# Kernel tuning notes

Hardware: AMD Instinct MI355X
Metric: run time of the kernel (lower is better)

## Reference

```python
import jax, jax.numpy as jnp
import numpy as np

N = 100000      # nodes
E = 1600000     # edges
G = 1024        # graphs in batch
NF = 9          # atom features (OGB AtomEncoder)
V = 128         # vocab per atom feature
H = 128         # hidden_dim
L = 3           # num_graph_layers
OUT = 10        # output_dim
BN_EPS = 1e-5


def setup_inputs() -> dict:
    key = jax.random.key(0)
    ks = jax.random.split(key, 12)
    x = jax.random.randint(ks[0], (N, NF), 0, V, dtype=jnp.int32)
    edge_index = jax.random.randint(ks[1], (2, E), 0, N, dtype=jnp.int32)
    batch = jnp.sort(jax.random.randint(ks[2], (N,), 0, G, dtype=jnp.int32))
    emb = jax.random.normal(ks[3], (NF, V, H), dtype=jnp.float32) * 0.05
    Ws = jax.random.normal(ks[4], (L, H, H), dtype=jnp.float32) * (1.0 / np.sqrt(H))
    bs = jnp.zeros((L, H), dtype=jnp.float32)
    gamma = jnp.ones((L - 1, H), dtype=jnp.float32)
    beta = jnp.zeros((L - 1, H), dtype=jnp.float32)
    run_mean = jax.random.normal(ks[5], (L - 1, H), dtype=jnp.float32) * 0.1
    run_var = jax.random.uniform(ks[6], (L - 1, H), minval=0.5, maxval=1.5, dtype=jnp.float32)
    W_clf = jax.random.normal(ks[7], (H, OUT), dtype=jnp.float32) * (1.0 / np.sqrt(H))
    b_clf = jnp.zeros((OUT,), dtype=jnp.float32)
    return {"x": x, "edge_index": edge_index, "batch": batch, "emb": emb,
            "Ws": Ws, "bs": bs, "gamma": gamma, "beta": beta,
            "run_mean": run_mean, "run_var": run_var,
            "W_clf": W_clf, "b_clf": b_clf}


def reference(x, edge_index, batch, emb, Ws, bs, gamma, beta, run_mean, run_var, W_clf, b_clf):
    # Eval-mode forward: dropout = identity, BatchNorm uses running stats.
    src, dst = edge_index[0], edge_index[1]
    # GCN symmetric normalization with self-loops: deg = 1 + in-degree
    deg = jax.ops.segment_sum(jnp.ones((E,), jnp.float32), dst, num_segments=N) + 1.0
    dinv = jax.lax.rsqrt(deg)                 # [N]
    norm_e = dinv[src] * dinv[dst]            # [E] edge coefficient
    norm_self = dinv * dinv                   # [N] self-loop coefficient

    # AtomEncoder: sum of per-feature embedding lookups -> [N, H]
    h = emb[jnp.arange(NF)[None, :], x].sum(axis=1)

    for i in range(L):
        hw = h @ Ws[i]                                                       # [N, H]
        h = (jax.ops.segment_sum(hw[src] * norm_e[:, None], dst, num_segments=N)
             + hw * norm_self[:, None] + bs[i])                              # GCNConv
        if i < L - 1:
            h = (h - run_mean[i]) * (gamma[i] * jax.lax.rsqrt(run_var[i] + BN_EPS)) + beta[i]
            h = jax.nn.relu(h)

    # global mean pool over graphs
    counts = jax.ops.segment_sum(jnp.ones((N,), jnp.float32), batch, num_segments=G)
    pooled = jax.ops.segment_sum(h, batch, num_segments=G) / jnp.maximum(counts, 1.0)[:, None]
    return pooled @ W_clf + b_clf             # [G, OUT]
```

## Files before the change

### kernel.cpp

```cpp
#include <hip/hip_runtime.h>
#include <hip/hip_bf16.h>
#include <hip/hip_fp16.h>

#define NN 100000
#define EE 1600000
#define GG 1024
#define NF 9
#define VV 128
#define HH 128
#define LL 3
#define OUTD 10
#define BN_EPS 1e-5f
#define NB_SCAN 98
#define NBUCK 196
#define BCAP 12288
#define CHUNK 4096
#define NB64 1563

typedef __attribute__((ext_vector_type(8))) short short8;
typedef __attribute__((ext_vector_type(8))) _Float16 half8;
typedef __attribute__((ext_vector_type(4))) float f32x4;

__device__ inline unsigned short f2bf(float x) {
    unsigned u = __float_as_uint(x);
    unsigned r = (u + 0x7fffu + ((u >> 16) & 1u)) >> 16;
    return (unsigned short)r;
}
__device__ inline float bf2f(unsigned short b) { return __uint_as_float(((unsigned)b) << 16); }

__device__ inline void mix8(float a[8], const uint4& r, float nm) {
    asm("v_fma_mix_f32 %0, %8, %12, %0 op_sel:[0,0,0] op_sel_hi:[1,0,0]\n\t"
        "v_fma_mix_f32 %1, %8, %12, %1 op_sel:[1,0,0] op_sel_hi:[1,0,0]\n\t"
        "v_fma_mix_f32 %2, %9, %12, %2 op_sel:[0,0,0] op_sel_hi:[1,0,0]\n\t"
        "v_fma_mix_f32 %3, %9, %12, %3 op_sel:[1,0,0] op_sel_hi:[1,0,0]\n\t"
        "v_fma_mix_f32 %4, %10, %12, %4 op_sel:[0,0,0] op_sel_hi:[1,0,0]\n\t"
        "v_fma_mix_f32 %5, %10, %12, %5 op_sel:[1,0,0] op_sel_hi:[1,0,0]\n\t"
        "v_fma_mix_f32 %6, %11, %12, %6 op_sel:[0,0,0] op_sel_hi:[1,0,0]\n\t"
        "v_fma_mix_f32 %7, %11, %12, %7 op_sel:[1,0,0] op_sel_hi:[1,0,0]"
        : "+v"(a[0]), "+v"(a[1]), "+v"(a[2]), "+v"(a[3]),
          "+v"(a[4]), "+v"(a[5]), "+v"(a[6]), "+v"(a[7])
        : "v"(r.x), "v"(r.y), "v"(r.z), "v"(r.w), "v"(nm));
}

__device__ inline void fma4(float4& a, const float4 r, float nm) {
    a.x = fmaf(r.x, nm, a.x); a.y = fmaf(r.y, nm, a.y);
    a.z = fmaf(r.z, nm, a.z); a.w = fmaf(r.w, nm, a.w);
}

__global__ __launch_bounds__(256) void split_kernel(const int* __restrict__ src,
                                                    const int* __restrict__ dst,
                                                    int* __restrict__ bcur,
                                                    int* __restrict__ bucket_edges) {
    __shared__ int lcnt[256], loff[256], lcur[256], gbase[256], sh[256];
    __shared__ int stage[CHUNK];
    __shared__ unsigned char stageb[CHUNK];
    int tid = threadIdx.x;
    int cs = blockIdx.x * CHUNK;
    int n = min(CHUNK, EE - cs);
    lcnt[tid] = 0;
    __syncthreads();
    for (int i = tid; i < n; i += 256)
        atomicAdd(&lcnt[dst[cs + i] >> 9], 1);
    __syncthreads();
    int val = lcnt[tid];
    sh[tid] = val; __syncthreads();
    for (int d = 1; d < 256; d <<= 1) {
        int t = (tid >= d) ? sh[tid - d] : 0;
        __syncthreads();
        sh[tid] += t;
        __syncthreads();
    }
    loff[tid] = sh[tid] - val;
    lcur[tid] = sh[tid] - val;
    __syncthreads();
    for (int i = tid; i < n; i += 256) {
        int d = dst[cs + i], s = src[cs + i];
        int b = d >> 9;
        int p = atomicAdd(&lcur[b], 1);
        stage[p] = (s << 9) | (d & 511);
        stageb[p] = (unsigned char)b;
    }
    if (val > 0) gbase[tid] = atomicAdd(&bcur[tid], val);
    __syncthreads();
    for (int i = tid; i < n; i += 256) {
        int b = stageb[i];
        bucket_edges[(size_t)b * BCAP + gbase[b] + (i - loff[b])] = stage[i];
    }
}

__global__ __launch_bounds__(256) void bhist_kernel(const int* __restrict__ bcur,
                                                    const int* __restrict__ bucket_edges,
                                                    int* __restrict__ cnt) {
    __shared__ int lc[512];
    int b = blockIdx.x, tid = threadIdx.x;
    lc[tid] = 0; lc[tid + 256] = 0;
    __syncthreads();
    int n = bcur[b];
    const int* be = bucket_edges + (size_t)b * BCAP;
    for (int i = tid; i < n; i += 256) atomicAdd(&lc[be[i] & 511], 1);
    __syncthreads();
    int node = b * 512 + tid;
    if (node < NN) cnt[node] = lc[tid];
    node += 256;
    if (node < NN) cnt[node] = lc[tid + 256];
}

__global__ void scanA_kernel(const int* __restrict__ cnt, int* __restrict__ bsum,
                             float* __restrict__ dinv) {
    __shared__ int sh[256];
    int tid = threadIdx.x;
    int base = blockIdx.x * 1024 + tid * 4;
    int s = 0;
#pragma unroll
    for (int i = 0; i < 4; ++i) {
        int idx = base + i;
        if (idx < NN) {
            int c = cnt[idx];
            s += c;
            dinv[idx] = rsqrtf(1.0f + (float)c);
        }
    }
    sh[tid] = s; __syncthreads();
    for (int d = 128; d > 0; d >>= 1) { if (tid < d) sh[tid] += sh[tid + d]; __syncthreads(); }
    if (tid == 0) bsum[blockIdx.x] = sh[0];
}

__global__ void scanB_kernel(int* __restrict__ bsum) {
    __shared__ int sh[128];
    int tid = threadIdx.x;
    int v = (tid < NB_SCAN) ? bsum[tid] : 0;
    sh[tid] = v; __syncthreads();
    for (int d = 1; d < 128; d <<= 1) {
        int t = (tid >= d) ? sh[tid - d] : 0;
        __syncthreads();
        sh[tid] += t;
        __syncthreads();
    }
    if (tid < NB_SCAN) bsum[tid] = sh[tid] - v;
}

__global__ void scanC_kernel(const int* __restrict__ cnt, const int* __restrict__ bsum,
                             int* __restrict__ row_ptr) {
    __shared__ int sh[256];
    int tid = threadIdx.x;
    int base = blockIdx.x * 1024 + tid * 4;
    int v[4];
#pragma unroll
    for (int i = 0; i < 4; ++i) { int idx = base + i; v[i] = (idx < NN) ? cnt[idx] : 0; }
    int tsum = v[0] + v[1] + v[2] + v[3];
    sh[tid] = tsum; __syncthreads();
    for (int d = 1; d < 256; d <<= 1) {
        int t = (tid >= d) ? sh[tid - d] : 0;
        __syncthreads();
        sh[tid] += t;
        __syncthreads();
    }
    int excl = sh[tid] - tsum + bsum[blockIdx.x];
#pragma unroll
    for (int i = 0; i < 4; ++i) {
        int idx = base + i;
        if (idx < NN) row_ptr[idx] = excl;
        excl += v[i];
    }
    if (blockIdx.x == 0 && tid == 0) row_ptr[NN] = EE;
}

__global__ __launch_bounds__(256) void cscatter_kernel(const int* __restrict__ bcur,
                                                       const int* __restrict__ bucket_edges,
                                                       const int* __restrict__ row_ptr,
                                                       const float* __restrict__ dinv,
                                                       int2* __restrict__ col) {
    __shared__ int lcur[512];
    int b = blockIdx.x, tid = threadIdx.x;
    int node0 = b * 512;
#pragma unroll
    for (int k = 0; k < 2; ++k) {
        int j = tid + k * 256;
        int node = node0 + j;
        if (node < NN) lcur[j] = row_ptr[node];
    }
    __syncthreads();
    int n = bcur[b];
    const int* be = bucket_edges + (size_t)b * BCAP;
    for (int i = tid; i < n; i += 256) {
        int w = be[i];
        int j = w & 511;
        int s = (int)((unsigned)w >> 9);
        int p = atomicAdd(&lcur[j], 1);
        float nm = dinv[s] * dinv[node0 + j];
        col[p] = make_int2(s, __float_as_int(nm));
    }
}

__global__ void wconv_kernel(const float* __restrict__ Ws,
                             unsigned short* __restrict__ WThi,
                             unsigned short* __restrict__ WTlo) {
    int id = blockIdx.x * 256 + threadIdx.x;
    if (id >= LL * HH * HH) return;
    int layer = id >> 14;
    int rem = id & (HH * HH - 1);
    int k = rem >> 7, n = rem & 127;
    float w = Ws[id];
    unsigned short hi = f2bf(w);
    float lo = w - bf2f(hi);
    WThi[(size_t)layer * HH * HH + n * HH + k] = hi;
    WTlo[(size_t)layer * HH * HH + n * HH + k] = f2bf(lo);
}

__global__ __launch_bounds__(256) void prep_clf_kernel(const float* __restrict__ Wc,
        const float* __restrict__ b2,
        _Float16* __restrict__ WcThi, _Float16* __restrict__ WcTlo,
        float* __restrict__ bb2) {
    int tid = threadIdx.x;
    for (int id = tid; id < 16 * HH; id += 256) {
        int n = id >> 7, k = id & 127;
        float w = (n < OUTD) ? Wc[k * OUTD + n] : 0.f;
        _Float16 hi = (_Float16)w;
        float lo = w - (float)hi;
        WcThi[id] = hi;
        WcTlo[id] = (_Float16)lo;
    }
    if (tid < OUTD) {
        float s = 0.f;
        for (int c = 0; c < HH; ++c) s += b2[c] * Wc[c * OUTD + tid];
        bb2[tid] = s;
    }
}

__global__ __launch_bounds__(256) void enc_mm_kernel(const int* __restrict__ x,
        const float* __restrict__ emb,
        const unsigned short* __restrict__ WThi, const unsigned short* __restrict__ WTlo,
        __half* __restrict__ hw_out) {
    __shared__ __align__(16) unsigned short lh[32][136];
    __shared__ __align__(16) unsigned short ll[32][136];
    int tid = threadIdx.x;
    int nloc = tid >> 3;
    int seg = tid & 7;
    int nodebase = blockIdx.x * 32;
    int n = nodebase + nloc;
    float s[16];
#pragma unroll
    for (int i = 0; i < 16; ++i) s[i] = 0.f;
#pragma unroll
    for (int f = 0; f < NF; ++f) {
        int idx = x[n * NF + f];
        const float4* ep = (const float4*)(emb + ((size_t)(f * VV + idx)) * HH + seg * 16);
#pragma unroll
        for (int q = 0; q < 4; ++q) {
            float4 e = ep[q];
            s[q * 4 + 0] += e.x; s[q * 4 + 1] += e.y;
            s[q * 4 + 2] += e.z; s[q * 4 + 3] += e.w;
        }
    }
#pragma unroll
    for (int q = 0; q < 4; ++q) {
        ushort4 oh, ol;
        oh.x = f2bf(s[q * 4 + 0]); ol.x = f2bf(s[q * 4 + 0] - bf2f(oh.x));
        oh.y = f2bf(s[q * 4 + 1]); ol.y = f2bf(s[q * 4 + 1] - bf2f(oh.y));
        oh.z = f2bf(s[q * 4 + 2]); ol.z = f2bf(s[q * 4 + 2] - bf2f(oh.z));
        oh.w = f2bf(s[q * 4 + 3]); ol.w = f2bf(s[q * 4 + 3] - bf2f(oh.w));
        *(ushort4*)&lh[nloc][seg * 16 + q * 4] = oh;
        *(ushort4*)&ll[nloc][seg * 16 + q * 4] = ol;
    }
    __syncthreads();
    int wave = tid >> 6, lane = tid & 63;
    int quad = lane >> 4, m = lane & 15;
    f32x4 acc[2][2] = {};
    int kq = quad * 8;
#pragma unroll
    for (int t = 0; t < 4; ++t) {
        int k0 = t * 32 + kq;
        short8 a0h = *(const short8*)&lh[m][k0];
        short8 a0l = *(const short8*)&ll[m][k0];
        short8 a1h = *(const short8*)&lh[16 + m][k0];
        short8 a1l = *(const short8*)&ll[16 + m][k0];
#pragma unroll
        for (int c = 0; c < 2; ++c) {
            int ct = wave * 2 + c;
            short8 bh = *(const short8*)(WThi + (size_t)(ct * 16 + m) * HH + k0);
            short8 bl = *(const short8*)(WTlo + (size_t)(ct * 16 + m) * HH + k0);
            acc[0][c] = __builtin_amdgcn_mfma_f32_16x16x32_bf16(a0h, bh, acc[0][c], 0, 0, 0);
            acc[0][c] = __builtin_amdgcn_mfma_f32_16x16x32_bf16(a0l, bh, acc[0][c], 0, 0, 0);
            acc[0][c] = __builtin_amdgcn_mfma_f32_16x16x32_bf16(a0h, bl, acc[0][c], 0, 0, 0);
            acc[1][c] = __builtin_amdgcn_mfma_f32_16x16x32_bf16(a1h, bh, acc[1][c], 0, 0, 0);
            acc[1][c] = __builtin_amdgcn_mfma_f32_16x16x32_bf16(a1l, bh, acc[1][c], 0, 0, 0);
            acc[1][c] = __builtin_amdgcn_mfma_f32_16x16x32_bf16(a1h, bl, acc[1][c], 0, 0, 0);
        }
    }
#pragma unroll
    for (int c = 0; c < 2; ++c) {
        int colx = (wave * 2 + c) * 16 + m;
#pragma unroll
        for (int rt = 0; rt < 2; ++rt) {
            int r0 = nodebase + rt * 16 + quad * 4;
#pragma unroll
            for (int reg = 0; reg < 4; ++reg)
                hw_out[(size_t)(r0 + reg) * HH + colx] = __float2half(acc[rt][c][reg]);
        }
    }
}

__device__ inline void gather_node(const uint4* __restrict__ hw4,
                                   const int2* __restrict__ col,
                                   int start, int end, int c4,
                                   float a[8], float b[8]) {
    int e = start;
    for (; e + 4 <= end; e += 4) {
        unsigned long long w0 = *(const unsigned long long*)&col[e];
        unsigned long long w1 = *(const unsigned long long*)&col[e + 1];
        unsigned long long w2 = *(const unsigned long long*)&col[e + 2];
        unsigned long long w3 = *(const unsigned long long*)&col[e + 3];
        uint4 r0 = hw4[(size_t)(unsigned)(w0 & 0xffffffffu) * 16 + c4];
        uint4 r1 = hw4[(size_t)(unsigned)(w1 & 0xffffffffu) * 16 + c4];
        uint4 r2 = hw4[(size_t)(unsigned)(w2 & 0xffffffffu) * 16 + c4];
        uint4 r3 = hw4[(size_t)(unsigned)(w3 & 0xffffffffu) * 16 + c4];
        mix8(a, r0, __int_as_float((int)(unsigned)(w0 >> 32)));
        mix8(b, r1, __int_as_float((int)(unsigned)(w1 >> 32)));
        mix8(a, r2, __int_as_float((int)(unsigned)(w2 >> 32)));
        mix8(b, r3, __int_as_float((int)(unsigned)(w3 >> 32)));
    }
    if (e < end) {
        int last = end - 1;
        int e1 = min(e + 1, last), e2 = min(e + 2, last), e3 = min(e + 3, last);
        unsigned long long w0 = *(const unsigned long long*)&col[e];
        unsigned long long w1 = *(const unsigned long long*)&col[e1];
        unsigned long long w2 = *(const unsigned long long*)&col[e2];
        unsigned long long w3 = *(const unsigned long long*)&col[e3];
        float n0 = __int_as_float((int)(unsigned)(w0 >> 32));
        float n1 = (e + 1 < end) ? __int_as_float((int)(unsigned)(w1 >> 32)) : 0.f;
        float n2 = (e + 2 < end) ? __int_as_float((int)(unsigned)(w2 >> 32)) : 0.f;
        float n3 = (e + 3 < end) ? __int_as_float((int)(unsigned)(w3 >> 32)) : 0.f;
        uint4 r0 = hw4[(size_t)(unsigned)(w0 & 0xffffffffu) * 16 + c4];
        uint4 r1 = hw4[(size_t)(unsigned)(w1 & 0xffffffffu) * 16 + c4];
        uint4 r2 = hw4[(size_t)(unsigned)(w2 & 0xffffffffu) * 16 + c4];
        uint4 r3 = hw4[(size_t)(unsigned)(w3 & 0xffffffffu) * 16 + c4];
        mix8(a, r0, n0);
        mix8(b, r1, n1);
        mix8(a, r2, n2);
        mix8(b, r3, n3);
    }
}

__global__ __launch_bounds__(512) void agg_mm_kernel(const __half* __restrict__ hw_in,
    const int* __restrict__ row_ptr, const int2* __restrict__ col,
    const float* __restrict__ dinv,
    const float* __restrict__ bias, const float* __restrict__ gamma,
    const float* __restrict__ beta, const float* __restrict__ rmean,
    const float* __restrict__ rvar,
    const unsigned short* __restrict__ WThi, const unsigned short* __restrict__ WTlo,
    __half* __restrict__ hw_out) {
    __shared__ __align__(16) unsigned short lh[32][136];
    __shared__ __align__(16) unsigned short ll[32][136];
    int wave = threadIdx.x >> 6;
    int lane = threadIdx.x & 63;
    int grp = lane >> 4;
    int c4 = lane & 15;
    int nodebase = blockIdx.x * 32;
    const uint4* hw4 = (const uint4*)hw_in;

    int v = nodebase + wave * 4 + grp;
    int start = row_ptr[v], end = row_ptr[v + 1];
    float a[8] = {}, b[8] = {};
    gather_node(hw4, col, start, end, c4, a, b);

    {
        float dv = dinv[v];
        uint4 r = hw4[(size_t)v * 16 + c4];
        mix8(a, r, dv * dv);
    }
#pragma unroll
    for (int i = 0; i < 8; ++i) a[i] += b[i];

    int ch = c4 * 8;
#pragma unroll
    for (int i = 0; i < 8; ++i) a[i] += bias[ch + i];
#pragma unroll
    for (int i = 0; i < 8; ++i) {
        int c = ch + i;
        float sc = gamma[c] * rsqrtf(rvar[c] + BN_EPS);
        a[i] = fmaxf((a[i] - rmean[c]) * sc + beta[c], 0.f);
    }
    int rloc = wave * 4 + grp;
    ushort4 oh0, oh1, ol0, ol1;
    oh0.x = f2bf(a[0]); ol0.x = f2bf(a[0] - bf2f(oh0.x));
    oh0.y = f2bf(a[1]); ol0.y = f2bf(a[1] - bf2f(oh0.y));
    oh0.z = f2bf(a[2]); ol0.z = f2bf(a[2] - bf2f(oh0.z));
    oh0.w = f2bf(a[3]); ol0.w = f2bf(a[3] - bf2f(oh0.w));
    oh1.x = f2bf(a[4]); ol1.x = f2bf(a[4] - bf2f(oh1.x));
    oh1.y = f2bf(a[5]); ol1.y = f2bf(a[5] - bf2f(oh1.y));
    oh1.z = f2bf(a[6]); ol1.z = f2bf(a[6] - bf2f(oh1.z));
    oh1.w = f2bf(a[7]); ol1.w = f2bf(a[7] - bf2f(oh1.w));
    *(ushort4*)&lh[rloc][ch]     = oh0;
    *(ushort4*)&lh[rloc][ch + 4] = oh1;
    *(ushort4*)&ll[rloc][ch]     = ol0;
    *(ushort4*)&ll[rloc][ch + 4] = ol1;

    __syncthreads();
    int quad = lane >> 4, m = lane & 15;
    f32x4 acc[2] = {};
    int kq = quad * 8;
    int ct = wave;
#pragma unroll
    for (int t = 0; t < 4; ++t) {
        int k0 = t * 32 + kq;
        short8 a0h = *(const short8*)&lh[m][k0];
        short8 a0l = *(const short8*)&ll[m][k0];
        short8 a1h = *(const short8*)&lh[16 + m][k0];
        short8 a1l = *(const short8*)&ll[16 + m][k0];
        short8 bh = *(const short8*)(WThi + (size_t)(ct * 16 + m) * HH + k0);
        short8 bl = *(const short8*)(WTlo + (size_t)(ct * 16 + m) * HH + k0);
        acc[0] = __builtin_amdgcn_mfma_f32_16x16x32_bf16(a0h, bh, acc[0], 0, 0, 0);
        acc[0] = __builtin_amdgcn_mfma_f32_16x16x32_bf16(a0l, bh, acc[0], 0, 0, 0);
        acc[0] = __builtin_amdgcn_mfma_f32_16x16x32_bf16(a0h, bl, acc[0], 0, 0, 0);
        acc[1] = __builtin_amdgcn_mfma_f32_16x16x32_bf16(a1h, bh, acc[1], 0, 0, 0);
        acc[1] = __builtin_amdgcn_mfma_f32_16x16x32_bf16(a1l, bh, acc[1], 0, 0, 0);
        acc[1] = __builtin_amdgcn_mfma_f32_16x16x32_bf16(a1h, bl, acc[1], 0, 0, 0);
    }
    int colx = ct * 16 + m;
#pragma unroll
    for (int rt = 0; rt < 2; ++rt) {
        int r0 = nodebase + rt * 16 + quad * 4;
#pragma unroll
        for (int reg = 0; reg < 4; ++reg)
            hw_out[(size_t)(r0 + reg) * HH + colx] = __float2half(acc[rt][reg]);
    }
}

__global__ __launch_bounds__(256) void yproj_kernel(const __half* __restrict__ hw_in,
        const _Float16* __restrict__ WcThi, const _Float16* __restrict__ WcTlo,
        float* __restrict__ y) {
    int tid = threadIdx.x;
    int wv = tid >> 6, lane = tid & 63;
    int quad = lane >> 4, m = lane & 15;
    int nodebase = blockIdx.x * 64 + wv * 16;
    int an = min(nodebase + m, NN - 1);
    f32x4 acc = {};
#pragma unroll
    for (int t = 0; t < 4; ++t) {
        int k0 = t * 32 + quad * 8;
        half8 a  = *(const half8*)(hw_in + (size_t)an * HH + k0);
        half8 bh = *(const half8*)(WcThi + m * HH + k0);
        half8 bl = *(const half8*)(WcTlo + m * HH + k0);
        acc = __builtin_amdgcn_mfma_f32_16x16x32_f16(a, bh, acc, 0, 0, 0);
        acc = __builtin_amdgcn_mfma_f32_16x16x32_f16(a, bl, acc, 0, 0, 0);
    }
#pragma unroll
    for (int reg = 0; reg < 4; ++reg) {
        int node = nodebase + quad * 4 + reg;
        if (node < NN) y[(size_t)node * 16 + m] = acc[reg];
    }
}

__global__ __launch_bounds__(256) void agg_pool10_kernel(const float* __restrict__ y,
    const int* __restrict__ row_ptr, const int2* __restrict__ col,
    const float* __restrict__ dinv, const int* __restrict__ batch,
    float* __restrict__ pooled) {
    __shared__ __align__(16) float lz[64][16];
    __shared__ int bg[64];
    int tid = threadIdx.x;
    int g4 = tid >> 2;
    int c = tid & 3;
    int nodebase = blockIdx.x * 64;
    int v = nodebase + g4;
    int vc = min(v, NN - 1);
    int start = row_ptr[vc];
    int end = (v < NN) ? row_ptr[vc + 1] : start;
    const float4* y4 = (const float4*)y;
    float4 a = {0.f, 0.f, 0.f, 0.f}, b = {0.f, 0.f, 0.f, 0.f};
    int e = start;
    for (; e + 4 <= end; e += 4) {
        unsigned long long w0 = *(const unsigned long long*)&col[e];
        unsigned long long w1 = *(const unsigned long long*)&col[e + 1];
        unsigned long long w2 = *(const unsigned long long*)&col[e + 2];
        unsigned long long w3 = *(const unsigned long long*)&col[e + 3];
        float4 r0 = y4[(size_t)(unsigned)(w0 & 0xffffffffu) * 4 + c];
        float4 r1 = y4[(size_t)(unsigned)(w1 & 0xffffffffu) * 4 + c];
        float4 r2 = y4[(size_t)(unsigned)(w2 & 0xffffffffu) * 4 + c];
        float4 r3 = y4[(size_t)(unsigned)(w3 & 0xffffffffu) * 4 + c];
        fma4(a, r0, __int_as_float((int)(unsigned)(w0 >> 32)));
        fma4(b, r1, __int_as_float((int)(unsigned)(w1 >> 32)));
        fma4(a, r2, __int_as_float((int)(unsigned)(w2 >> 32)));
        fma4(b, r3, __int_as_float((int)(unsigned)(w3 >> 32)));
    }
    if (e < end) {
        int last = end - 1;
        int e1 = min(e + 1, last), e2 = min(e + 2, last), e3 = min(e + 3, last);
        unsigned long long w0 = *(const unsigned long long*)&col[e];
        unsigned long long w1 = *(const unsigned long long*)&col[e1];
        unsigned long long w2 = *(const unsigned long long*)&col[e2];
        unsigned long long w3 = *(const unsigned long long*)&col[e3];
        float n0 = __int_as_float((int)(unsigned)(w0 >> 32));
        float n1 = (e + 1 < end) ? __int_as_float((int)(unsigned)(w1 >> 32)) : 0.f;
        float n2 = (e + 2 < end) ? __int_as_float((int)(unsigned)(w2 >> 32)) : 0.f;
        float n3 = (e + 3 < end) ? __int_as_float((int)(unsigned)(w3 >> 32)) : 0.f;
        float4 r0 = y4[(size_t)(unsigned)(w0 & 0xffffffffu) * 4 + c];
        float4 r1 = y4[(size_t)(unsigned)(w1 & 0xffffffffu) * 4 + c];
        float4 r2 = y4[(size_t)(unsigned)(w2 & 0xffffffffu) * 4 + c];
        float4 r3 = y4[(size_t)(unsigned)(w3 & 0xffffffffu) * 4 + c];
        fma4(a, r0, n0);
        fma4(b, r1, n1);
        fma4(a, r2, n2);
        fma4(b, r3, n3);
    }
    if (v < NN) {
        float dv = dinv[v];
        float4 r = y4[(size_t)v * 4 + c];
        fma4(a, r, dv * dv);
    }
    a.x += b.x; a.y += b.y; a.z += b.z; a.w += b.w;
    *(float4*)&lz[g4][c * 4] = a;
    if (c == 0) bg[g4] = batch[vc];
    __syncthreads();
    int ch = tid & 15;
    int rh = tid >> 4;
    int r0i = rh * 4;
    int curg = bg[r0i];
    float run = 0.f;
    for (int r = r0i; r < r0i + 4; ++r) {
        int gg = bg[r];
        if (gg != curg) {
            atomicAdd(&pooled[(size_t)curg * 16 + ch], run);
            run = 0.f; curg = gg;
        }
        run += lz[r][ch];
    }
    atomicAdd(&pooled[(size_t)curg * 16 + ch], run);
}

__global__ __launch_bounds__(256) void finalize_kernel(const float* __restrict__ pooled,
    const int* __restrict__ batch, const float* __restrict__ bb2,
    const float* __restrict__ bc, float* __restrict__ out) {
    int id = blockIdx.x * 256 + threadIdx.x;
    if (id >= GG * 16) return;
    int g = id >> 4, o = id & 15;
    if (o >= OUTD) return;
    int lo = 0, hi = NN;
    while (lo < hi) { int mid = (lo + hi) >> 1; if (batch[mid] < g) lo = mid + 1; else hi = mid; }
    int s0 = lo;
    lo = 0; hi = NN;
    int g1 = g + 1;
    while (lo < hi) { int mid = (lo + hi) >> 1; if (batch[mid] < g1) lo = mid + 1; else hi = mid; }
    int cnt = lo - s0;
    float r = pooled[(size_t)g * 16 + o] / fmaxf((float)cnt, 1.0f);
    out[(size_t)g * OUTD + o] = r + ((cnt > 0) ? bb2[o] : 0.f) + bc[o];
}

extern "C" void kernel_launch(void* const* d_in, const int* in_sizes, int n_in,
                              void* d_out, int out_size, void* d_ws, size_t ws_size,
                              hipStream_t stream) {
    const int*   x      = (const int*)d_in[0];
    const int*   eidx   = (const int*)d_in[1];
    const int*   batch  = (const int*)d_in[2];
    const float* emb    = (const float*)d_in[3];
    const float* Ws     = (const float*)d_in[4];
    const float* bs     = (const float*)d_in[5];
    const float* gamma  = (const float*)d_in[6];
    const float* beta   = (const float*)d_in[7];
    const float* rmean  = (const float*)d_in[8];
    const float* rvar   = (const float*)d_in[9];
    const float* Wclf   = (const float*)d_in[10];
    const float* bclf   = (const float*)d_in[11];
    float* out = (float*)d_out;

    const int* e_src = eidx;
    const int* e_dst = eidx + EE;

    char* ws = (char*)d_ws;
    size_t off = 0;
    auto take = [&](size_t bytes) -> void* {
        void* p = ws + off;
        off = (off + bytes + 255) & ~(size_t)255;
        return p;
    };
    float* dinv     = (float*)take((size_t)NN * 4);
    int*   cnt      = (int*)  take((size_t)NN * 4);
    int*   row_ptr  = (int*)  take((size_t)(NN + 1) * 4);
    int*   bsum     = (int*)  take((size_t)NB_SCAN * 4);
    int*   bcur     = (int*)  take((size_t)256 * 4);
    int*   bucket_edges = (int*)take((size_t)NBUCK * BCAP * 4);
    int2*  col      = (int2*) take((size_t)EE * 8);
    __half* hwA     = (__half*)take((size_t)NN * HH * 2);
    __half* hwB     = (__half*)take((size_t)NN * HH * 2);
    float* y        = (float*)take((size_t)NN * 16 * 4);
    float* pooled   = (float*)take((size_t)GG * 16 * 4);
    unsigned short* WThi = (unsigned short*)take((size_t)LL * HH * HH * 2);
    unsigned short* WTlo = (unsigned short*)take((size_t)LL * HH * HH * 2);
    _Float16* WcThi = (_Float16*)take((size_t)16 * HH * 2);
    _Float16* WcTlo = (_Float16*)take((size_t)16 * HH * 2);
    float* bb2      = (float*)take((size_t)16 * 4);

    hipMemsetAsync(bcur, 0, 256 * 4, stream);
    hipMemsetAsync(pooled, 0, (size_t)GG * 16 * 4, stream);

    split_kernel<<<(EE + CHUNK - 1) / CHUNK, 256, 0, stream>>>(e_src, e_dst, bcur, bucket_edges);
    bhist_kernel<<<NBUCK, 256, 0, stream>>>(bcur, bucket_edges, cnt);
    scanA_kernel<<<NB_SCAN, 256, 0, stream>>>(cnt, bsum, dinv);
    scanB_kernel<<<1, 128, 0, stream>>>(bsum);
    scanC_kernel<<<NB_SCAN, 256, 0, stream>>>(cnt, bsum, row_ptr);
    cscatter_kernel<<<NBUCK, 256, 0, stream>>>(bcur, bucket_edges, row_ptr, dinv, col);
    wconv_kernel<<<(LL * HH * HH + 255) / 256, 256, 0, stream>>>(Ws, WThi, WTlo);
    prep_clf_kernel<<<1, 256, 0, stream>>>(Wclf, bs + 2 * HH, WcThi, WcTlo, bb2);

    enc_mm_kernel<<<NN / 32, 256, 0, stream>>>(x, emb, WThi, WTlo, hwA);
    agg_mm_kernel<<<NN / 32, 512, 0, stream>>>(hwA, row_ptr, col, dinv,
        bs, gamma, beta, rmean, rvar,
        WThi + (size_t)1 * HH * HH, WTlo + (size_t)1 * HH * HH, hwB);
    agg_mm_kernel<<<NN / 32, 512, 0, stream>>>(hwB, row_ptr, col, dinv,
        bs + HH, gamma + HH, beta + HH, rmean + HH, rvar + HH,
        WThi + (size_t)2 * HH * HH, WTlo + (size_t)2 * HH * HH, hwA);
    yproj_kernel<<<NB64, 256, 0, stream>>>(hwA, WcThi, WcTlo, y);
    agg_pool10_kernel<<<NB64, 256, 0, stream>>>(y, row_ptr, col, dinv, batch, pooled);
    finalize_kernel<<<(GG * 16 + 255) / 256, 256, 0, stream>>>(pooled, batch, bb2, bclf, out);
}
```

Baseline: 412.0 us.

## Fuse classifier projection into last GCN layer and store projected features in fp16

```diff
diff --git a/kernel.cpp b/kernel.cpp
--- a/kernel.cpp
+++ b/kernel.cpp
@@ -11,14 +11,12 @@
 #define LL 3
 #define OUTD 10
 #define BN_EPS 1e-5f
-#define NB_SCAN 98
 #define NBUCK 196
 #define BCAP 12288
 #define CHUNK 4096
-#define NB64 1563
+#define NB128 782
 
 typedef __attribute__((ext_vector_type(8))) short short8;
-typedef __attribute__((ext_vector_type(8))) _Float16 half8;
 typedef __attribute__((ext_vector_type(4))) float f32x4;
 
 __device__ inline unsigned short f2bf(float x) {
@@ -42,11 +40,6 @@
         : "v"(r.x), "v"(r.y), "v"(r.z), "v"(r.w), "v"(nm));
 }
 
-__device__ inline void fma4(float4& a, const float4 r, float nm) {
-    a.x = fmaf(r.x, nm, a.x); a.y = fmaf(r.y, nm, a.y);
-    a.z = fmaf(r.z, nm, a.z); a.w = fmaf(r.w, nm, a.w);
-}
-
 __global__ __launch_bounds__(256) void split_kernel(const int* __restrict__ src,
                                                     const int* __restrict__ dst,
                                                     int* __restrict__ bcur,
@@ -90,8 +83,11 @@
 
 __global__ __launch_bounds__(256) void bhist_kernel(const int* __restrict__ bcur,
                                                     const int* __restrict__ bucket_edges,
-                                                    int* __restrict__ cnt) {
+                                                    int* __restrict__ cnt,
+                                                    float* __restrict__ dinv,
+                                                    int* __restrict__ bsum) {
     __shared__ int lc[512];
+    __shared__ int sh[256];
     int b = blockIdx.x, tid = threadIdx.x;
     lc[tid] = 0; lc[tid + 256] = 0;
     __syncthreads();
@@ -100,68 +96,47 @@
     for (int i = tid; i < n; i += 256) atomicAdd(&lc[be[i] & 511], 1);
     __syncthreads();
     int node = b * 512 + tid;
-    if (node < NN) cnt[node] = lc[tid];
-    node += 256;
-    if (node < NN) cnt[node] = lc[tid + 256];
-}
-
-__global__ void scanA_kernel(const int* __restrict__ cnt, int* __restrict__ bsum,
-                             float* __restrict__ dinv) {
+    int c0 = lc[tid], c1 = lc[tid + 256];
+    int s = 0;
+    if (node < NN) { cnt[node] = c0; dinv[node] = rsqrtf(1.0f + (float)c0); s += c0; }
+    if (node + 256 < NN) { cnt[node + 256] = c1; dinv[node + 256] = rsqrtf(1.0f + (float)c1); s += c1; }
+    sh[tid] = s; __syncthreads();
+    for (int d = 128; d > 0; d >>= 1) { if (tid < d) sh[tid] += sh[tid + d]; __syncthreads(); }
+    if (tid == 0) bsum[b] = sh[0];
+}
+
+__global__ void scanB_kernel(int* __restrict__ bsum) {
     __shared__ int sh[256];
     int tid = threadIdx.x;
-    int base = blockIdx.x * 1024 + tid * 4;
-    int s = 0;
-#pragma unroll
-    for (int i = 0; i < 4; ++i) {
-        int idx = base + i;
-        if (idx < NN) {
-            int c = cnt[idx];
-            s += c;
-            dinv[idx] = rsqrtf(1.0f + (float)c);
-        }
-    }
-    sh[tid] = s; __syncthreads();
-    for (int d = 128; d > 0; d >>= 1) { if (tid < d) sh[tid] += sh[tid + d]; __syncthreads(); }
-    if (tid == 0) bsum[blockIdx.x] = sh[0];
-}
-
-__global__ void scanB_kernel(int* __restrict__ bsum) {
-    __shared__ int sh[128];
-    int tid = threadIdx.x;
-    int v = (tid < NB_SCAN) ? bsum[tid] : 0;
+    int v = (tid < NBUCK) ? bsum[tid] : 0;
     sh[tid] = v; __syncthreads();
-    for (int d = 1; d < 128; d <<= 1) {
-        int t = (tid >= d) ? sh[tid - d] : 0;
-        __syncthreads();
-        sh[tid] += t;
-        __syncthreads();
-    }
-    if (tid < NB_SCAN) bsum[tid] = sh[tid] - v;
-}
-
-__global__ void scanC_kernel(const int* __restrict__ cnt, const int* __restrict__ bsum,
-                             int* __restrict__ row_ptr) {
-    __shared__ int sh[256];
-    int tid = threadIdx.x;
-    int base = blockIdx.x * 1024 + tid * 4;
-    int v[4];
-#pragma unroll
-    for (int i = 0; i < 4; ++i) { int idx = base + i; v[i] = (idx < NN) ? cnt[idx] : 0; }
-    int tsum = v[0] + v[1] + v[2] + v[3];
-    sh[tid] = tsum; __syncthreads();
     for (int d = 1; d < 256; d <<= 1) {
         int t = (tid >= d) ? sh[tid - d] : 0;
         __syncthreads();
         sh[tid] += t;
         __syncthreads();
     }
-    int excl = sh[tid] - tsum + bsum[blockIdx.x];
-#pragma unroll
-    for (int i = 0; i < 4; ++i) {
-        int idx = base + i;
-        if (idx < NN) row_ptr[idx] = excl;
-        excl += v[i];
-    }
+    if (tid < NBUCK) bsum[tid] = sh[tid] - v;
+}
+
+__global__ void scanC_kernel(const int* __restrict__ cnt, const int* __restrict__ bsum,
+                             int* __restrict__ row_ptr) {
+    __shared__ int sh[256];
+    int tid = threadIdx.x;
+    int base = blockIdx.x * 512 + tid * 2;
+    int v0 = (base < NN) ? cnt[base] : 0;
+    int v1 = (base + 1 < NN) ? cnt[base + 1] : 0;
+    int ts = v0 + v1;
+    sh[tid] = ts; __syncthreads();
+    for (int d = 1; d < 256; d <<= 1) {
+        int t = (tid >= d) ? sh[tid - d] : 0;
+        __syncthreads();
+        sh[tid] += t;
+        __syncthreads();
+    }
+    int excl = sh[tid] - ts + bsum[blockIdx.x];
+    if (base < NN) row_ptr[base] = excl;
+    if (base + 1 < NN) row_ptr[base + 1] = excl + v0;
     if (blockIdx.x == 0 && tid == 0) row_ptr[NN] = EE;
 }
 
@@ -192,38 +167,41 @@
     }
 }
 
-__global__ void wconv_kernel(const float* __restrict__ Ws,
-                             unsigned short* __restrict__ WThi,
-                             unsigned short* __restrict__ WTlo) {
+__global__ __launch_bounds__(256) void wprep_kernel(const float* __restrict__ Ws,
+        const float* __restrict__ Wc, const float* __restrict__ b2,
+        unsigned short* __restrict__ WThi, unsigned short* __restrict__ WTlo,
+        unsigned short* __restrict__ WcThi, unsigned short* __restrict__ WcTlo,
+        float* __restrict__ bb2) {
     int id = blockIdx.x * 256 + threadIdx.x;
-    if (id >= LL * HH * HH) return;
-    int layer = id >> 14;
-    int rem = id & (HH * HH - 1);
-    int k = rem >> 7, n = rem & 127;
-    float w = Ws[id];
-    unsigned short hi = f2bf(w);
-    float lo = w - bf2f(hi);
-    WThi[(size_t)layer * HH * HH + n * HH + k] = hi;
-    WTlo[(size_t)layer * HH * HH + n * HH + k] = f2bf(lo);
-}
-
-__global__ __launch_bounds__(256) void prep_clf_kernel(const float* __restrict__ Wc,
-        const float* __restrict__ b2,
-        _Float16* __restrict__ WcThi, _Float16* __restrict__ WcTlo,
-        float* __restrict__ bb2) {
-    int tid = threadIdx.x;
-    for (int id = tid; id < 16 * HH; id += 256) {
-        int n = id >> 7, k = id & 127;
-        float w = (n < OUTD) ? Wc[k * OUTD + n] : 0.f;
-        _Float16 hi = (_Float16)w;
-        float lo = w - (float)hi;
-        WcThi[id] = hi;
-        WcTlo[id] = (_Float16)lo;
-    }
-    if (tid < OUTD) {
-        float s = 0.f;
-        for (int c = 0; c < HH; ++c) s += b2[c] * Wc[c * OUTD + tid];
-        bb2[tid] = s;
+    if (id < LL * HH * HH) {
+        int layer = id >> 14;
+        int rem = id & (HH * HH - 1);
+        int k = rem >> 7, n = rem & 127;
+        float w = Ws[id];
+        unsigned short hi = f2bf(w);
+        float lo = w - bf2f(hi);
+        WThi[(size_t)layer * HH * HH + n * HH + k] = hi;
+        WTlo[(size_t)layer * HH * HH + n * HH + k] = f2bf(lo);
+    }
+    if (blockIdx.x == 0) {
+        int tid = threadIdx.x;
+        const float* W2 = Ws + (size_t)2 * HH * HH;
+        for (int i = tid; i < 16 * HH; i += 256) {
+            int n = i >> 7, k = i & 127;
+            float s = 0.f;
+            if (n < OUTD) {
+                for (int j = 0; j < HH; ++j)
+                    s += W2[k * HH + j] * Wc[j * OUTD + n];
+            }
+            unsigned short hi = f2bf(s);
+            WcThi[i] = hi;
+            WcTlo[i] = f2bf(s - bf2f(hi));
+        }
+        if (tid < OUTD) {
+            float s = 0.f;
+            for (int c = 0; c < HH; ++c) s += b2[c] * Wc[c * OUTD + tid];
+            bb2[tid] = s;
+        }
     }
 }
 
@@ -341,6 +319,7 @@
     }
 }
 
+template<bool DO_PROJ>
 __global__ __launch_bounds__(512) void agg_mm_kernel(const __half* __restrict__ hw_in,
     const int* __restrict__ row_ptr, const int2* __restrict__ col,
     const float* __restrict__ dinv,
@@ -348,7 +327,9 @@
     const float* __restrict__ beta, const float* __restrict__ rmean,
     const float* __restrict__ rvar,
     const unsigned short* __restrict__ WThi, const unsigned short* __restrict__ WTlo,
-    __half* __restrict__ hw_out) {
+    __half* __restrict__ hw_out,
+    const unsigned short* __restrict__ WcThi, const unsigned short* __restrict__ WcTlo,
+    __half* __restrict__ y_out) {
     __shared__ __align__(16) unsigned short lh[32][136];
     __shared__ __align__(16) unsigned short ll[32][136];
     int wave = threadIdx.x >> 6;
@@ -424,63 +405,60 @@
         for (int reg = 0; reg < 4; ++reg)
             hw_out[(size_t)(r0 + reg) * HH + colx] = __float2half(acc[rt][reg]);
     }
-}
-
-__global__ __launch_bounds__(256) void yproj_kernel(const __half* __restrict__ hw_in,
-        const _Float16* __restrict__ WcThi, const _Float16* __restrict__ WcTlo,
-        float* __restrict__ y) {
-    int tid = threadIdx.x;
-    int wv = tid >> 6, lane = tid & 63;
-    int quad = lane >> 4, m = lane & 15;
-    int nodebase = blockIdx.x * 64 + wv * 16;
-    int an = min(nodebase + m, NN - 1);
-    f32x4 acc = {};
-#pragma unroll
-    for (int t = 0; t < 4; ++t) {
-        int k0 = t * 32 + quad * 8;
-        half8 a  = *(const half8*)(hw_in + (size_t)an * HH + k0);
-        half8 bh = *(const half8*)(WcThi + m * HH + k0);
-        half8 bl = *(const half8*)(WcTlo + m * HH + k0);
-        acc = __builtin_amdgcn_mfma_f32_16x16x32_f16(a, bh, acc, 0, 0, 0);
-        acc = __builtin_amdgcn_mfma_f32_16x16x32_f16(a, bl, acc, 0, 0, 0);
-    }
-#pragma unroll
-    for (int reg = 0; reg < 4; ++reg) {
-        int node = nodebase + quad * 4 + reg;
-        if (node < NN) y[(size_t)node * 16 + m] = acc[reg];
-    }
-}
-
-__global__ __launch_bounds__(256) void agg_pool10_kernel(const float* __restrict__ y,
+
+    if constexpr (DO_PROJ) {
+        if (wave < 2) {
+            f32x4 pacc = {};
+#pragma unroll
+            for (int t = 0; t < 4; ++t) {
+                int k0 = t * 32 + kq;
+                short8 ah = *(const short8*)&lh[wave * 16 + m][k0];
+                short8 al = *(const short8*)&ll[wave * 16 + m][k0];
+                short8 bh = *(const short8*)(WcThi + (size_t)m * HH + k0);
+                short8 bl = *(const short8*)(WcTlo + (size_t)m * HH + k0);
+                pacc = __builtin_amdgcn_mfma_f32_16x16x32_bf16(ah, bh, pacc, 0, 0, 0);
+                pacc = __builtin_amdgcn_mfma_f32_16x16x32_bf16(al, bh, pacc, 0, 0, 0);
+                pacc = __builtin_amdgcn_mfma_f32_16x16x32_bf16(ah, bl, pacc, 0, 0, 0);
+            }
+#pragma unroll
+            for (int reg = 0; reg < 4; ++reg) {
+                int node = nodebase + wave * 16 + quad * 4 + reg;
+                y_out[(size_t)node * 16 + m] = __float2half(pacc[reg]);
+            }
+        }
+    }
+}
+
+__global__ __launch_bounds__(256) void agg_pool_kernel(const __half* __restrict__ y,
     const int* __restrict__ row_ptr, const int2* __restrict__ col,
     const float* __restrict__ dinv, const int* __restrict__ batch,
     float* __restrict__ pooled) {
-    __shared__ __align__(16) float lz[64][16];
-    __shared__ int bg[64];
+    __shared__ __align__(16) float lz[128][16];
+    __shared__ int bg[128];
     int tid = threadIdx.x;
-    int g4 = tid >> 2;
-    int c = tid & 3;
-    int nodebase = blockIdx.x * 64;
-    int v = nodebase + g4;
+    int g2 = tid >> 1;
+    int cl = tid & 1;
+    int nodebase = blockIdx.x * 128;
+    int v = nodebase + g2;
     int vc = min(v, NN - 1);
     int start = row_ptr[vc];
     int end = (v < NN) ? row_ptr[vc + 1] : start;
-    const float4* y4 = (const float4*)y;
-    float4 a = {0.f, 0.f, 0.f, 0.f}, b = {0.f, 0.f, 0.f, 0.f};
+    const uint4* y4 = (const uint4*)y;
+    float a[8] = {};
     int e = start;
     for (; e + 4 <= end; e += 4) {
         unsigned long long w0 = *(const unsigned long long*)&col[e];
         unsigned long long w1 = *(const unsigned long long*)&col[e + 1];
         unsigned long long w2 = *(const unsigned long long*)&col[e + 2];
         unsigned long long w3 = *(const unsigned long long*)&col[e + 3];
-        float4 r0 = y4[(size_t)(unsigned)(w0 & 0xffffffffu) * 4 + c];
-        float4 r1 = y4[(size_t)(unsigned)(w1 & 0xffffffffu) * 4 + c];
-        float4 r2 = y4[(size_t)(unsigned)(w2 & 0xffffffffu) * 4 + c];
-        float4 r3 = y4[(size_t)(unsigned)(w3 & 0xffffffffu) * 4 + c];
-        fma4(a, r0, __int_as_float((int)(unsigned)(w0 >> 32)));
-        fma4(b, r1, __int_as_float((int)(unsigned)(w1 >> 32)));
-        fma4(a, r2, __int_as_float((int)(unsigned)(w2 >> 32)));
-        fma4(b, r3, __int_as_float((int)(unsigned)(w3 >> 32)));
+        uint4 r0 = y4[(size_t)(unsigned)(w0 & 0xffffffffu) * 2 + cl];
+        uint4 r1 = y4[(size_t)(unsigned)(w1 & 0xffffffffu) * 2 + cl];
+        uint4 r2 = y4[(size_t)(unsigned)(w2 & 0xffffffffu) * 2 + cl];
+        uint4 r3 = y4[(size_t)(unsigned)(w3 & 0xffffffffu) * 2 + cl];
+        mix8(a, r0, __int_as_float((int)(unsigned)(w0 >> 32)));
+        mix8(a, r1, __int_as_float((int)(unsigned)(w1 >> 32)));
+        mix8(a, r2, __int_as_float((int)(unsigned)(w2 >> 32)));
+        mix8(a, r3, __int_as_float((int)(unsigned)(w3 >> 32)));
     }
     if (e < end) {
         int last = end - 1;
@@ -493,30 +471,34 @@
         float n1 = (e + 1 < end) ? __int_as_float((int)(unsigned)(w1 >> 32)) : 0.f;
         float n2 = (e + 2 < end) ? __int_as_float((int)(unsigned)(w2 >> 32)) : 0.f;
         float n3 = (e + 3 < end) ? __int_as_float((int)(unsigned)(w3 >> 32)) : 0.f;
-        float4 r0 = y4[(size_t)(unsigned)(w0 & 0xffffffffu) * 4 + c];
-        float4 r1 = y4[(size_t)(unsigned)(w1 & 0xffffffffu) * 4 + c];
-        float4 r2 = y4[(size_t)(unsigned)(w2 & 0xffffffffu) * 4 + c];
-        float4 r3 = y4[(size_t)(unsigned)(w3 & 0xffffffffu) * 4 + c];
-        fma4(a, r0, n0);
-        fma4(b, r1, n1);
-        fma4(a, r2, n2);
-        fma4(b, r3, n3);
+        uint4 r0 = y4[(size_t)(unsigned)(w0 & 0xffffffffu) * 2 + cl];
+        uint4 r1 = y4[(size_t)(unsigned)(w1 & 0xffffffffu) * 2 + cl];
+        uint4 r2 = y4[(size_t)(unsigned)(w2 & 0xffffffffu) * 2 + cl];
+        uint4 r3 = y4[(size_t)(unsigned)(w3 & 0xffffffffu) * 2 + cl];
+        mix8(a, r0, n0);
+        mix8(a, r1, n1);
+        mix8(a, r2, n2);
+        mix8(a, r3, n3);
     }
     if (v < NN) {
         float dv = dinv[v];
-        float4 r = y4[(size_t)v * 4 + c];
-        fma4(a, r, dv * dv);
-    }
-    a.x += b.x; a.y += b.y; a.z += b.z; a.w += b.w;
-    *(float4*)&lz[g4][c * 4] = a;
-    if (c == 0) bg[g4] = batch[vc];
+        uint4 r = y4[(size_t)v * 2 + cl];
+        mix8(a, r, dv * dv);
+    } else {
+#pragma unroll
+        for (int i = 0; i < 8; ++i) a[i] = 0.f;
+    }
+    int chb = cl * 8;
+#pragma unroll
+    for (int i = 0; i < 8; ++i) lz[g2][chb + i] = a[i];
+    if (cl == 0) bg[g2] = batch[vc];
     __syncthreads();
     int ch = tid & 15;
     int rh = tid >> 4;
-    int r0i = rh * 4;
+    int r0i = rh * 8;
     int curg = bg[r0i];
     float run = 0.f;
-    for (int r = r0i; r < r0i + 4; ++r) {
+    for (int r = r0i; r < r0i + 8; ++r) {
         int gg = bg[r];
         if (gg != curg) {
             atomicAdd(&pooled[(size_t)curg * 16 + ch], run);
@@ -575,40 +557,40 @@
     float* dinv     = (float*)take((size_t)NN * 4);
     int*   cnt      = (int*)  take((size_t)NN * 4);
     int*   row_ptr  = (int*)  take((size_t)(NN + 1) * 4);
-    int*   bsum     = (int*)  take((size_t)NB_SCAN * 4);
+    int*   bsum     = (int*)  take((size_t)NBUCK * 4);
     int*   bcur     = (int*)  take((size_t)256 * 4);
     int*   bucket_edges = (int*)take((size_t)NBUCK * BCAP * 4);
-    int2*  col      = (int2*) take((size_t)EE * 8);
+    int2*  col      = (int2*) take((size_t)EE * 8 + 64);
     __half* hwA     = (__half*)take((size_t)NN * HH * 2);
     __half* hwB     = (__half*)take((size_t)NN * HH * 2);
-    float* y        = (float*)take((size_t)NN * 16 * 4);
+    __half* yh      = (__half*)take((size_t)NN * 16 * 2);
     float* pooled   = (float*)take((size_t)GG * 16 * 4);
     unsigned short* WThi = (unsigned short*)take((size_t)LL * HH * HH * 2);
     unsigned short* WTlo = (unsigned short*)take((size_t)LL * HH * HH * 2);
-    _Float16* WcThi = (_Float16*)take((size_t)16 * HH * 2);
-    _Float16* WcTlo = (_Float16*)take((size_t)16 * HH * 2);
+    unsigned short* WcThi = (unsigned short*)take((size_t)16 * HH * 2);
+    unsigned short* WcTlo = (unsigned short*)take((size_t)16 * HH * 2);
     float* bb2      = (float*)take((size_t)16 * 4);
 
     hipMemsetAsync(bcur, 0, 256 * 4, stream);
     hipMemsetAsync(pooled, 0, (size_t)GG * 16 * 4, stream);
 
     split_kernel<<<(EE + CHUNK - 1) / CHUNK, 256, 0, stream>>>(e_src, e_dst, bcur, bucket_edges);
-    bhist_kernel<<<NBUCK, 256, 0, stream>>>(bcur, bucket_edges, cnt);
-    scanA_kernel<<<NB_SCAN, 256, 0, stream>>>(cnt, bsum, dinv);
-    scanB_kernel<<<1, 128, 0, stream>>>(bsum);
-    scanC_kernel<<<NB_SCAN, 256, 0, stream>>>(cnt, bsum, row_ptr);
+    bhist_kernel<<<NBUCK, 256, 0, stream>>>(bcur, bucket_edges, cnt, dinv, bsum);
+    scanB_kernel<<<1, 256, 0, stream>>>(bsum);
+    scanC_kernel<<<NBUCK, 256, 0, stream>>>(cnt, bsum, row_ptr);
     cscatter_kernel<<<NBUCK, 256, 0, stream>>>(bcur, bucket_edges, row_ptr, dinv, col);
-    wconv_kernel<<<(LL * HH * HH + 255) / 256, 256, 0, stream>>>(Ws, WThi, WTlo);
-    prep_clf_kernel<<<1, 256, 0, stream>>>(Wclf, bs + 2 * HH, WcThi, WcTlo, bb2);
+    wprep_kernel<<<(LL * HH * HH + 255) / 256, 256, 0, stream>>>(Ws, Wclf, bs + 2 * HH,
+        WThi, WTlo, WcThi, WcTlo, bb2);
 
     enc_mm_kernel<<<NN / 32, 256, 0, stream>>>(x, emb, WThi, WTlo, hwA);
-    agg_mm_kernel<<<NN / 32, 512, 0, stream>>>(hwA, row_ptr, col, dinv,
+    agg_mm_kernel<false><<<NN / 32, 512, 0, stream>>>(hwA, row_ptr, col, dinv,
         bs, gamma, beta, rmean, rvar,
-        WThi + (size_t)1 * HH * HH, WTlo + (size_t)1 * HH * HH, hwB);
-    agg_mm_kernel<<<NN / 32, 512, 0, stream>>>(hwB, row_ptr, col, dinv,
+        WThi + (size_t)1 * HH * HH, WTlo + (size_t)1 * HH * HH, hwB,
+        nullptr, nullptr, nullptr);
+    agg_mm_kernel<true><<<NN / 32, 512, 0, stream>>>(hwB, row_ptr, col, dinv,
         bs + HH, gamma + HH, beta + HH, rmean + HH, rvar + HH,
-        WThi + (size_t)2 * HH * HH, WTlo + (size_t)2 * HH * HH, hwA);
-    yproj_kernel<<<NB64, 256, 0, stream>>>(hwA, WcThi, WcTlo, y);
-    agg_pool10_kernel<<<NB64, 256, 0, stream>>>(y, row_ptr, col, dinv, batch, pooled);
+        WThi + (size_t)2 * HH * HH, WTlo + (size_t)2 * HH * HH, hwA,
+        WcThi, WcTlo, yh);
+    agg_pool_kernel<<<NB128, 256, 0, stream>>>(yh, row_ptr, col, dinv, batch, pooled);
     finalize_kernel<<<(GG * 16 + 255) / 256, 256, 0, stream>>>(pooled, batch, bb2, bclf, out);
 }
```

Result: no change. 411.2 us (-0.2%).
